# Kernel optimization log

Hardware: AMD Instinct MI355X
Metric: run time of the kernel (lower is better)

The kernel has to match this reference:

```python
import jax, jax.numpy as jnp
import numpy as np

# Faithful translation of SIMPLE.imputate:
#   - first loop sets `last` to the LAST observed (mask<0.9) value in the row
#     (wrap-around initialization)
#   - second loop forward-fills: missing (mask>0.9) positions get `last`,
#     observed positions update `last`.
# Equivalent vectorized form: cummax of observed indices (forward-fill index),
# with leading missing positions falling back to the last observed index in the
# row, then a single gather.

def setup_inputs() -> dict:
    key = jax.random.key(0)
    k1, k2 = jax.random.split(key)
    B, N, D = 64, 4096, 128
    inp = jax.random.normal(k1, (B, N, D), dtype=jnp.float32)
    mask = jax.random.uniform(k2, (B, N), dtype=jnp.float32)  # >0.9 => missing
    return {"input": inp, "mask": mask}


def reference(input, mask):
    b, n, d = input.shape
    observed = mask < 0.9                       # [b, n] True where value is kept
    j = jnp.arange(n, dtype=jnp.int32)
    obs_idx = jnp.where(observed, j, jnp.int32(-1))           # [b, n]
    # index of most recent observed position <= j (inclusive cummax)
    ff_idx = jax.lax.associative_scan(jnp.maximum, obs_idx, axis=1)
    # wrap-around init: leading missing positions use the row's last observed idx
    last_overall = jnp.max(obs_idx, axis=1, keepdims=True)    # [b, 1]
    gather_idx = jnp.where(ff_idx < 0, last_overall, ff_idx)  # [b, n]
    gather_idx = jnp.maximum(gather_idx, 0)  # guard: row with no observed values
    out = jnp.take_along_axis(input, gather_idx[:, :, None], axis=1)  # [b, n, d]
    return out
```

## Files before the change

kernel.cpp:

```cpp
#include <hip/hip_runtime.h>


#define FF_N 4096
#define FF_D 128

__global__ __launch_bounds__(256) void ffill_scan(const float* __restrict__ mask,
                                                  int* __restrict__ gidx) {
    const int N = FF_N;
    const int PER = 16;
    const int b = blockIdx.x;
    const float* m = mask + (size_t)b * N;
    int* g = gidx + (size_t)b * N;
    const int tid = threadIdx.x;
    const int base = tid * PER;

    float4 mv[4];
    const float4* m4 = reinterpret_cast<const float4*>(m + base);
#pragma unroll
    for (int k = 0; k < 4; ++k) mv[k] = m4[k];

    unsigned obsbits = 0;
    int segmax = -1;
#pragma unroll
    for (int k = 0; k < 4; ++k) {
        const float vals[4] = {mv[k].x, mv[k].y, mv[k].z, mv[k].w};
#pragma unroll
        for (int j = 0; j < 4; ++j) {
            const int idx = k * 4 + j;
            const bool o = vals[j] < 0.9f;
            obsbits |= (unsigned)o << idx;
            if (o) segmax = base + idx;
        }
    }

    __shared__ int smem[256];
    smem[tid] = segmax;
    __syncthreads();
    int v = segmax;
#pragma unroll
    for (int off = 1; off < 256; off <<= 1) {
        const int t = (tid >= off) ? smem[tid - off] : -1;
        __syncthreads();
        v = max(v, t);
        smem[tid] = v;
        __syncthreads();
    }
    const int prefix = tid ? smem[tid - 1] : -1;
    const int total  = smem[255];
    const int fallback = (total < 0) ? 0 : total;

    int outv[16];
    int last = prefix;
#pragma unroll
    for (int k = 0; k < PER; ++k) {
        if ((obsbits >> k) & 1u) last = base + k;
        outv[k] = (last < 0) ? fallback : last;
    }

    int4* g4 = reinterpret_cast<int4*>(g + base);
#pragma unroll
    for (int k = 0; k < 4; ++k)
        g4[k] = make_int4(outv[4 * k], outv[4 * k + 1], outv[4 * k + 2], outv[4 * k + 3]);
}

__global__ __launch_bounds__(256) void ffill_gather(const float4* __restrict__ in,
                                                    const int* __restrict__ gidx,
                                                    float4* __restrict__ out,
                                                    int total4) {
    const int stride = gridDim.x * blockDim.x;
    for (int q = blockIdx.x * blockDim.x + threadIdx.x; q < total4; q += stride) {
        const int row = q >> 5;
        const int l   = q & 31;
        const int gi  = gidx[row];
        const int srow = (row & ~(FF_N - 1)) + gi;
        out[q] = in[(size_t)srow * (FF_D / 4) + l];
    }
}

extern "C" void kernel_launch(void* const* d_in, const int* in_sizes, int n_in,
                              void* d_out, int out_size, void* d_ws, size_t ws_size,
                              hipStream_t stream) {
    const float* inp  = (const float*)d_in[0];
    const float* mask = (const float*)d_in[1];
    float* out = (float*)d_out;

    const int B = in_sizes[1] / FF_N;
    int* gidx = (int*)d_ws;

    ffill_scan<<<B, 256, 0, stream>>>(mask, gidx);

    const int total4 = B * FF_N * (FF_D / 4);
    ffill_gather<<<2048, 256, 0, stream>>>(
        (const float4*)inp, gidx, (float4*)out, total4);
}
```

Baseline: 233.8 us.

## Fuse forward-fill scan and gather into one kernel with per-slice redundant scan

```diff
diff --git a/kernel.cpp b/kernel.cpp
--- a/kernel.cpp
+++ b/kernel.cpp
@@ -3,16 +3,21 @@
 
 #define FF_N 4096
 #define FF_D 128
+#define SLICES 32
+#define SLICE_N (FF_N / SLICES)
 
-__global__ __launch_bounds__(256) void ffill_scan(const float* __restrict__ mask,
-                                                  int* __restrict__ gidx) {
-    const int N = FF_N;
-    const int PER = 16;
-    const int b = blockIdx.x;
-    const float* m = mask + (size_t)b * N;
-    int* g = gidx + (size_t)b * N;
+__global__ __launch_bounds__(256) void ffill_fused(const float4* __restrict__ in,
+                                                   const float* __restrict__ mask,
+                                                   float4* __restrict__ out) {
+    const int b   = blockIdx.x >> 5;
+    const int s   = blockIdx.x & 31;
     const int tid = threadIdx.x;
-    const int base = tid * PER;
+
+    __shared__ int gidx[FF_N];
+    __shared__ int scanbuf[256];
+
+    const float* m = mask + (size_t)b * FF_N;
+    const int base = tid * 16;
 
     float4 mv[4];
     const float4* m4 = reinterpret_cast<const float4*>(m + base);
@@ -33,47 +38,46 @@
         }
     }
 
-    __shared__ int smem[256];
-    smem[tid] = segmax;
+    scanbuf[tid] = segmax;
     __syncthreads();
     int v = segmax;
 #pragma unroll
     for (int off = 1; off < 256; off <<= 1) {
-        const int t = (tid >= off) ? smem[tid - off] : -1;
+        const int t = (tid >= off) ? scanbuf[tid - off] : -1;
         __syncthreads();
         v = max(v, t);
-        smem[tid] = v;
+        scanbuf[tid] = v;
         __syncthreads();
     }
-    const int prefix = tid ? smem[tid - 1] : -1;
-    const int total  = smem[255];
+    const int prefix   = tid ? scanbuf[tid - 1] : -1;
+    const int total    = scanbuf[255];
     const int fallback = (total < 0) ? 0 : total;
 
+    int last = prefix;
     int outv[16];
-    int last = prefix;
 #pragma unroll
-    for (int k = 0; k < PER; ++k) {
+    for (int k = 0; k < 16; ++k) {
         if ((obsbits >> k) & 1u) last = base + k;
         outv[k] = (last < 0) ? fallback : last;
     }
-
-    int4* g4 = reinterpret_cast<int4*>(g + base);
+    int4* g4 = reinterpret_cast<int4*>(&gidx[base]);
 #pragma unroll
     for (int k = 0; k < 4; ++k)
         g4[k] = make_int4(outv[4 * k], outv[4 * k + 1], outv[4 * k + 2], outv[4 * k + 3]);
-}
+    __syncthreads();
 
-__global__ __launch_bounds__(256) void ffill_gather(const float4* __restrict__ in,
-                                                    const int* __restrict__ gidx,
-                                                    float4* __restrict__ out,
-                                                    int total4) {
-    const int stride = gridDim.x * blockDim.x;
-    for (int q = blockIdx.x * blockDim.x + threadIdx.x; q < total4; q += stride) {
-        const int row = q >> 5;
-        const int l   = q & 31;
-        const int gi  = gidx[row];
-        const int srow = (row & ~(FF_N - 1)) + gi;
-        out[q] = in[(size_t)srow * (FF_D / 4) + l];
+    const size_t rowbase = (size_t)b * FF_N * (FF_D / 4);
+    const float4* inb  = in  + rowbase;
+    float4*       outb = out + rowbase + (size_t)s * SLICE_N * (FF_D / 4);
+    const int nbase = s * SLICE_N;
+
+#pragma unroll
+    for (int p = 0; p < 16; ++p) {
+        const int q    = p * 256 + tid;
+        const int nloc = q >> 5;
+        const int l    = q & 31;
+        const int gi   = gidx[nbase + nloc];
+        outb[q] = inb[(size_t)gi * (FF_D / 4) + l];
     }
 }
 
@@ -85,11 +89,6 @@
     float* out = (float*)d_out;
 
     const int B = in_sizes[1] / FF_N;
-    int* gidx = (int*)d_ws;
-
-    ffill_scan<<<B, 256, 0, stream>>>(mask, gidx);
-
-    const int total4 = B * FF_N * (FF_D / 4);
-    ffill_gather<<<2048, 256, 0, stream>>>(
-        (const float4*)inp, gidx, (float4*)out, total4);
+    ffill_fused<<<B * SLICES, 256, 0, stream>>>(
+        (const float4*)inp, mask, (float4*)out);
 }
```

After: 236.1 us. Within noise of the previous version (+1.0%).

## Use wave shuffles for scan and batch gather loads with nontemporal stores

Applied to the files above, without the earlier changes.

```diff
diff --git a/kernel.cpp b/kernel.cpp
--- a/kernel.cpp
+++ b/kernel.cpp
@@ -4,15 +4,15 @@
 #define FF_N 4096
 #define FF_D 128
 
+typedef float f4 __attribute__((ext_vector_type(4)));
+
 __global__ __launch_bounds__(256) void ffill_scan(const float* __restrict__ mask,
                                                   int* __restrict__ gidx) {
-    const int N = FF_N;
-    const int PER = 16;
     const int b = blockIdx.x;
-    const float* m = mask + (size_t)b * N;
-    int* g = gidx + (size_t)b * N;
-    const int tid = threadIdx.x;
-    const int base = tid * PER;
+    const float* m = mask + (size_t)b * FF_N;
+    int* g = gidx + (size_t)b * FF_N;
+    const int tid  = threadIdx.x;
+    const int base = tid * 16;
 
     float4 mv[4];
     const float4* m4 = reinterpret_cast<const float4*>(m + base);
@@ -33,48 +33,64 @@
         }
     }
 
-    __shared__ int smem[256];
-    smem[tid] = segmax;
+    const int lane = tid & 63;
+    int incl = segmax;
+#pragma unroll
+    for (int off = 1; off < 64; off <<= 1) {
+        const int t = __shfl_up(incl, off, 64);
+        if (lane >= off) incl = max(incl, t);
+    }
+
+    __shared__ int wmax[4];
+    if (lane == 63) wmax[tid >> 6] = incl;
     __syncthreads();
-    int v = segmax;
+    const int wid = tid >> 6;
+    int wpre = -1, total = -1;
 #pragma unroll
-    for (int off = 1; off < 256; off <<= 1) {
-        const int t = (tid >= off) ? smem[tid - off] : -1;
-        __syncthreads();
-        v = max(v, t);
-        smem[tid] = v;
-        __syncthreads();
+    for (int w = 0; w < 4; ++w) {
+        const int x = wmax[w];
+        total = max(total, x);
+        if (w < wid) wpre = max(wpre, x);
     }
-    const int prefix = tid ? smem[tid - 1] : -1;
-    const int total  = smem[255];
+    const int inclp  = __shfl_up(incl, 1, 64);
+    const int prefix = max(wpre, (lane == 0) ? -1 : inclp);
     const int fallback = (total < 0) ? 0 : total;
 
+    int last = prefix;
     int outv[16];
-    int last = prefix;
 #pragma unroll
-    for (int k = 0; k < PER; ++k) {
+    for (int k = 0; k < 16; ++k) {
         if ((obsbits >> k) & 1u) last = base + k;
         outv[k] = (last < 0) ? fallback : last;
     }
-
     int4* g4 = reinterpret_cast<int4*>(g + base);
 #pragma unroll
     for (int k = 0; k < 4; ++k)
         g4[k] = make_int4(outv[4 * k], outv[4 * k + 1], outv[4 * k + 2], outv[4 * k + 3]);
 }
 
-__global__ __launch_bounds__(256) void ffill_gather(const float4* __restrict__ in,
+__global__ __launch_bounds__(256) void ffill_gather(const f4* __restrict__ in,
                                                     const int* __restrict__ gidx,
-                                                    float4* __restrict__ out,
-                                                    int total4) {
-    const int stride = gridDim.x * blockDim.x;
-    for (int q = blockIdx.x * blockDim.x + threadIdx.x; q < total4; q += stride) {
-        const int row = q >> 5;
-        const int l   = q & 31;
-        const int gi  = gidx[row];
-        const int srow = (row & ~(FF_N - 1)) + gi;
-        out[q] = in[(size_t)srow * (FF_D / 4) + l];
-    }
+                                                    f4* __restrict__ out) {
+    const int rowblk = blockIdx.x << 6;
+    const int tid  = threadIdx.x;
+    const int lane = tid & 31;
+    const int rsub = tid >> 5;
+
+    int gi[8];
+#pragma unroll
+    for (int i = 0; i < 8; ++i) gi[i] = gidx[rowblk + i * 8 + rsub];
+
+    const int bbase = rowblk & ~(FF_N - 1);
+    f4 v[8];
+#pragma unroll
+    for (int i = 0; i < 8; ++i)
+        v[i] = in[(size_t)(bbase + gi[i]) * (FF_D / 4) + lane];
+
+    const size_t ob = (size_t)rowblk * (FF_D / 4);
+#pragma unroll
+    for (int i = 0; i < 8; ++i)
+        __builtin_nontemporal_store(v[i], &out[ob + i * 256 + tid]);
 }
 
 extern "C" void kernel_launch(void* const* d_in, const int* in_sizes, int n_in,
@@ -82,14 +98,11 @@
                               hipStream_t stream) {
     const float* inp  = (const float*)d_in[0];
     const float* mask = (const float*)d_in[1];
-    float* out = (float*)d_out;
+    f4* out = (f4*)d_out;
 
     const int B = in_sizes[1] / FF_N;
     int* gidx = (int*)d_ws;
 
     ffill_scan<<<B, 256, 0, stream>>>(mask, gidx);
-
-    const int total4 = B * FF_N * (FF_D / 4);
-    ffill_gather<<<2048, 256, 0, stream>>>(
-        (const float4*)inp, gidx, (float4*)out, total4);
+    ffill_gather<<<(B * FF_N) / 64, 256, 0, stream>>>((const f4*)inp, gidx, out);
 }
```

After: 236.3 us. About the same (+1.1%).
